# Optimization experiments

Measured on AMD Instinct MI355X. Metric: run time of the kernel, lower is better.

The kernel has to match this reference:

```python
import jax, jax.numpy as jnp
import numpy as np

D_MODEL = 1024
N_HEADS = 16
D_K = D_MODEL // N_HEADS
THETA = 10000.0
MAX_SEQ = 2048


def _trunc_normal(key, shape, std):
    # approximate trunc_normal in [-3std, 3std] via clipping (init only; values irrelevant to math)
    return jnp.clip(jax.random.normal(key, shape) * std, -3 * std, 3 * std).astype(jnp.float32)


def setup_inputs() -> dict:
    key = jax.random.key(0)
    kx, kq, kk, kv, ko = jax.random.split(key, 5)
    std = np.sqrt(2.0 / (D_MODEL + D_MODEL))
    x = jax.random.normal(kx, (2, 2048, D_MODEL), dtype=jnp.float32)
    W_q = _trunc_normal(kq, (D_MODEL, D_MODEL), std)
    W_k = _trunc_normal(kk, (D_MODEL, D_MODEL), std)
    W_v = _trunc_normal(kv, (D_MODEL, D_MODEL), std)
    W_o = _trunc_normal(ko, (D_MODEL, D_MODEL), std)
    return {"x": x, "W_q": W_q, "W_k": W_k, "W_v": W_v, "W_o": W_o}


def _rope(x, positions):
    # x: [b, n, s, d_k]; interleaved even/odd pairing: (x0,x1),(x2,x3),...
    d = x.shape[-1]
    inv_freq = THETA ** (-2.0 * jnp.arange(0, d // 2, dtype=jnp.float32) / d)
    angles = positions.astype(jnp.float32)[:, None] * inv_freq[None, :]  # [s, d/2]
    cos, sin = jnp.cos(angles), jnp.sin(angles)
    xp = x.reshape(x.shape[:-1] + (d // 2, 2))
    x_even, x_odd = xp[..., 0], xp[..., 1]
    out_even = x_even * cos - x_odd * sin
    out_odd = x_even * sin + x_odd * cos
    return jnp.stack((out_even, out_odd), axis=-1).reshape(x.shape)


def reference(x, W_q, W_k, W_v, W_o):
    b, s, _ = x.shape
    def split_heads(t):
        return t.reshape(b, s, N_HEADS, D_K).transpose(0, 2, 1, 3)  # b n s d
    Q = split_heads(x @ W_q.T)
    K = split_heads(x @ W_k.T)
    V = split_heads(x @ W_v.T)
    pos = jnp.arange(s)
    Q = _rope(Q, pos)
    K = _rope(K, pos)
    score = jnp.einsum('bnqd,bnkd->bnqk', Q, K) / jnp.sqrt(jnp.float32(D_K))
    causal = jnp.triu(jnp.ones((s, s), dtype=bool), k=1)
    score = jnp.where(causal[None, None], -jnp.inf, score)
    attn = jax.nn.softmax(score, axis=-1)
    out = jnp.einsum('bnqk,bnkd->bnqd', attn, V)
    out = out.transpose(0, 2, 1, 3).reshape(b, s, D_MODEL)
    return out @ W_o.T
```

## Files before the change

### kernel.cpp

```cpp
#include <hip/hip_runtime.h>

typedef float f32x4 __attribute__((ext_vector_type(4)));
typedef __bf16 bf16x8 __attribute__((ext_vector_type(8)));

#define D_MODEL 1024
#define SEQ     2048
#define NB      2
#define NH      16
#define DK      64

__device__ __forceinline__ unsigned short f2bf(float f) {
    union { float f; unsigned int u; } un; un.f = f;
    unsigned int r = un.u + 0x7fffu + ((un.u >> 16) & 1u);
    return (unsigned short)(r >> 16);
}

__device__ __forceinline__ unsigned cvtpk(float lo, float hi) {
    unsigned r;
    asm("v_cvt_pk_bf16_f32 %0, %1, %2" : "=v"(r) : "v"(lo), "v"(hi));
    return r;
}

__device__ __forceinline__ void gload16(const void* g, void* l) {
    __builtin_amdgcn_global_load_lds((__attribute__((address_space(1))) void*)g,
                                     (__attribute__((address_space(3))) void*)l,
                                     16, 0, 0);
}

__global__ __launch_bounds__(256) void cast5(
    const float* __restrict__ x,  const float* __restrict__ wq,
    const float* __restrict__ wk, const float* __restrict__ wv,
    const float* __restrict__ wo,
    unsigned short* __restrict__ xb,  unsigned short* __restrict__ wqb,
    unsigned short* __restrict__ wkb, unsigned short* __restrict__ wvb,
    unsigned short* __restrict__ wob, float2* __restrict__ tab)
{
    if (blockIdx.y == 5) {
        int idx = blockIdx.x * 256 + threadIdx.x;
        if (idx < SEQ * 32) {
            int ss = idx >> 5, p = idx & 31;
            float freq = exp2f(-0.41524101186f * (float)p);
            float sn, cs;
            sincosf((float)ss * freq, &sn, &cs);
            tab[idx] = make_float2(cs, sn);
        }
        return;
    }
    const float* src; unsigned short* dst; int n8;
    switch (blockIdx.y) {
        case 0:  src = x;  dst = xb;  n8 = (NB*SEQ*D_MODEL)/8; break;
        case 1:  src = wq; dst = wqb; n8 = (D_MODEL*D_MODEL)/8; break;
        case 2:  src = wk; dst = wkb; n8 = (D_MODEL*D_MODEL)/8; break;
        case 3:  src = wv; dst = wvb; n8 = (D_MODEL*D_MODEL)/8; break;
        default: src = wo; dst = wob; n8 = (D_MODEL*D_MODEL)/8; break;
    }
    int stride = gridDim.x * blockDim.x;
    for (int i = blockIdx.x * blockDim.x + threadIdx.x; i < n8; i += stride) {
        const float4* p = (const float4*)src + (size_t)i * 2;
        float4 a = p[0], b = p[1];
        union { unsigned short h[8]; uint4 v; } u;
        u.h[0] = f2bf(a.x); u.h[1] = f2bf(a.y); u.h[2] = f2bf(a.z); u.h[3] = f2bf(a.w);
        u.h[4] = f2bf(b.x); u.h[5] = f2bf(b.y); u.h[6] = f2bf(b.z); u.h[7] = f2bf(b.w);
        ((uint4*)dst)[i] = u.v;
    }
}

template <int MODE, int BM, int BN>
__global__ __launch_bounds__(256) void gemm_bt(
    const unsigned short* __restrict__ A,
    const unsigned short* __restrict__ B0,
    const unsigned short* __restrict__ B1,
    const unsigned short* __restrict__ B2,
    float* __restrict__ outF,
    unsigned short* __restrict__ Qh,
    unsigned short* __restrict__ Kh,
    unsigned short* __restrict__ Vt,
    const float2* __restrict__ tab,
    int M, int K)
{
    constexpr int PER_STAGE = (BM + BN) / 64;
    constexpr int WM = BM / 2, WN = BN / 2;
    constexpr int FM = WM / 16, FN = WN / 16;
    __shared__ __align__(16) unsigned short SM[3 * (BM + BN) * 32];

    const int lane = threadIdx.x & 63;
    const int wid  = threadIdx.x >> 6;
    const int l15 = lane & 15, lhi = lane >> 4;

    const int L  = blockIdx.x;
    const int yl = L & 7;
    const int t  = L >> 3;
    const int bx = t & 7;
    const int t2 = t >> 3;
    int y, z;
    if constexpr (MODE == 1) { y = ((t2 & 3) << 3) | yl; z = t2 >> 2; }
    else                     { y = (t2 << 3) | yl;       z = 0;       }
    const int m0 = y * BM;
    const int n0 = bx * BN;
    const unsigned short* B = (z == 0) ? B0 : (z == 1) ? B1 : B2;
    const int waveM = (wid >> 1) * WM;
    const int waveN = (wid & 1) * WN;

    f32x4 acc[FM][FN];
    f32x4 zero = {0.f, 0.f, 0.f, 0.f};
#pragma unroll
    for (int m = 0; m < FM; ++m)
#pragma unroll
        for (int n = 0; n < FN; ++n) acc[m][n] = zero;

    const int lrow = lane >> 2;
    const int uslot = lane & 3;

    auto STAGE = [&](int buf, int k0) {
        unsigned short* as = SM + buf * (BM + BN) * 32;
        unsigned short* bs = as + BM * 32;
#pragma unroll
        for (int q = 0; q < BM / 64; ++q) {
            int rbase = wid * (BM / 4) + q * 16;
            int r = rbase + lrow;
            int ug = (uslot - (r >> 1)) & 3;
            gload16(A + (size_t)(m0 + r) * K + k0 + ug * 8,
                    (char*)as + rbase * 64);
        }
#pragma unroll
        for (int q = 0; q < BN / 64; ++q) {
            int rbase = wid * (BN / 4) + q * 16;
            int r = rbase + lrow;
            int ug = (uslot - (r >> 1)) & 3;
            gload16(B + (size_t)(n0 + r) * K + k0 + ug * 8,
                    (char*)bs + rbase * 64);
        }
    };

    const int NK = K >> 5;
    STAGE(0, 0);
    STAGE(1, 32);

    for (int k = 0; k < NK; ++k) {
        if (k < NK - 1) {
            if constexpr (PER_STAGE == 4) asm volatile("s_waitcnt vmcnt(4)" ::: "memory");
            else                          asm volatile("s_waitcnt vmcnt(3)" ::: "memory");
        } else {
            asm volatile("s_waitcnt vmcnt(0)" ::: "memory");
        }
        __builtin_amdgcn_s_barrier();
        __builtin_amdgcn_sched_barrier(0);
        if (k + 2 < NK) STAGE((k + 2) % 3, (k + 2) << 5);

        const unsigned short* as = SM + (k % 3) * (BM + BN) * 32;
        const unsigned short* bs = as + BM * 32;
        bf16x8 af[FM], bfr[FN];
#pragma unroll
        for (int m = 0; m < FM; ++m) {
            int ra = waveM + m * 16 + l15;
            af[m] = *(const bf16x8*)(as + ra * 32 + (((lhi + (ra >> 1)) & 3) << 3));
        }
#pragma unroll
        for (int n = 0; n < FN; ++n) {
            int rb = waveN + n * 16 + l15;
            bfr[n] = *(const bf16x8*)(bs + rb * 32 + (((lhi + (rb >> 1)) & 3) << 3));
        }
        __builtin_amdgcn_s_setprio(1);
#pragma unroll
        for (int m = 0; m < FM; ++m)
#pragma unroll
            for (int n = 0; n < FN; ++n)
                acc[m][n] = __builtin_amdgcn_mfma_f32_16x16x32_bf16(af[m], bfr[n], acc[m][n], 0, 0, 0);
        __builtin_amdgcn_s_setprio(0);
    }

    if constexpr (MODE == 0) {
#pragma unroll
        for (int n = 0; n < FN; ++n) {
            int col = n0 + waveN + n * 16 + l15;
#pragma unroll
            for (int m = 0; m < FM; ++m) {
                int rowb = m0 + waveM + m * 16 + (lhi << 2);
#pragma unroll
                for (int r = 0; r < 4; ++r)
                    outF[(size_t)(rowb + r) * D_MODEL + col] = acc[m][n][r];
            }
        }
    } else {
        __syncthreads();
        unsigned short* Ct = ((unsigned short*)SM) + wid * 4608;
        const int colg0 = n0 + waveN;
        const int hh    = (colg0 >> 6) & (NH - 1);
        const int rowg0 = m0 + waveM;
        const int bb    = rowg0 >> 11;
        const size_t bhh = (size_t)(bb * NH + hh);

#pragma unroll
        for (int n = 0; n < 4; ++n) {
            int cl = n * 16 + l15;
#pragma unroll
            for (int m = 0; m < 4; ++m) {
#pragma unroll
                for (int r = 0; r < 4; ++r) {
                    float v  = acc[m][n][r];
                    float pv = __shfl_xor(v, 1);
                    int rl = m * 16 + (lhi << 2) + r;
                    if (z == 2) {
                        Ct[cl * 72 + rl] = f2bf(v);
                    } else {
                        int ss = (rowg0 + rl) & (SEQ - 1);
                        float2 cs = tab[(ss << 5) + (cl >> 1)];
                        float o = (cl & 1) ? (pv * cs.y + v * cs.x)
                                           : (v * cs.x - pv * cs.y);
                        if (z == 0) o *= 0.18033688011f;
                        Ct[rl * 72 + cl] = f2bf(o);
                    }
                }
            }
        }
        asm volatile("s_waitcnt lgkmcnt(0)" ::: "memory");

        const int lr = lane >> 3;
        const int lc = (lane & 7) << 3;
#pragma unroll
        for (int i = 0; i < 8; ++i) {
            int rl = i * 8 + lr;
            uint4 w = *(const uint4*)&Ct[rl * 72 + lc];
            if (z == 2) {
                int ss0 = rowg0 & (SEQ - 1);
                *(uint4*)(Vt + (bhh * DK + rl) * SEQ + ss0 + lc) = w;
            } else {
                int ss = (rowg0 + rl) & (SEQ - 1);
                unsigned short* dst = (z == 0) ? Qh : Kh;
                *(uint4*)(dst + (bhh * SEQ + ss) * DK + lc) = w;
            }
        }
    }
}

__global__ __launch_bounds__(256) void attn_kernel(
    const unsigned short* __restrict__ Qh,
    const unsigned short* __restrict__ Kh,
    const unsigned short* __restrict__ Vt,
    unsigned short* __restrict__ O)
{
    __shared__ unsigned short Ks[3][64 * 64];
    __shared__ unsigned short Vs[3][64 * 64];
    __shared__ unsigned short P[4][16 * 64];

    const int tid  = threadIdx.x;
    const int lane = tid & 63;
    const int wid  = tid >> 6;
    const int l15 = lane & 15, lhi = lane >> 4;

    const int L   = blockIdx.x;
    const int xcd = L & 7;
    const int r0  = L >> 3;
    const int bh  = (xcd << 2) | (r0 & 3);
    const int pi  = r0 >> 2;
    const int b = bh >> 4, h = bh & 15;

    const unsigned short* Qb = Qh + (size_t)bh * SEQ * DK;
    const unsigned short* Kb = Kh + (size_t)bh * SEQ * DK;
    const unsigned short* Vb = Vt + (size_t)bh * DK * SEQ;

    const int NT0 = pi + 1;
    const int NTT = 33;

    auto kv_of = [&](int g) { return (g < NT0 ? g : g - NT0) << 6; };

    auto STAGE = [&](int buf, int kv0s) {
#pragma unroll
        for (int c = 0; c < 2; ++c) {
            int ub = c * 256 + wid * 64;
            int u  = ub + lane;
            int kr = u >> 3;
            int kc = (u & 7) ^ (kr & 7);
            gload16(Kb + (size_t)(kv0s + kr) * DK + kc * 8, &Ks[buf][(size_t)ub * 8]);
            gload16(Vb + (size_t)kr * SEQ + kv0s + kc * 8, &Vs[buf][(size_t)ub * 8]);
        }
    };

    const f32x4 zero = {0.f, 0.f, 0.f, 0.f};
    const f32x4 ninf = {-1e30f, -1e30f, -1e30f, -1e30f};
    const int sw = l15 & 7;

    STAGE(0, 0);
    STAGE(1, kv_of(1));
    int g = 0;

    for (int ph = 0; ph < 2; ++ph) {
        const int qt = ph ? (31 - pi) : pi;
        const int q0 = qt << 6;
        const int qw = q0 + wid * 16;
        const int lastkt = qt;

        bf16x8 qf[2];
#pragma unroll
        for (int kk = 0; kk < 2; ++kk)
            qf[kk] = *(const bf16x8*)(Qb + (size_t)(qw + l15) * DK + kk * 32 + lhi * 8);

        f32x4 oacc[4];
#pragma unroll
        for (int nd = 0; nd < 4; ++nd) oacc[nd] = zero;
        float mrow = -1e30f;
        float lrow = 0.f;

        for (int kt = 0; kt <= lastkt; ++kt, ++g) {
            const int kv0 = kt << 6;
            const bool diag = (kt == lastkt);
            const int nlim = diag ? (wid + 1) : 4;

            if (g < NTT - 1) asm volatile("s_waitcnt vmcnt(4)" ::: "memory");
            else             asm volatile("s_waitcnt vmcnt(0)" ::: "memory");
            __builtin_amdgcn_s_barrier();
            __builtin_amdgcn_sched_barrier(0);
            if (g + 2 < NTT) STAGE((g + 2) % 3, kv_of(g + 2));

            const unsigned short* Kc = Ks[g % 3];
            const unsigned short* Vc = Vs[g % 3];

            f32x4 s[4];
#pragma unroll
            for (int n = 0; n < 4; ++n) s[n] = (n < nlim) ? zero : ninf;

            __builtin_amdgcn_s_setprio(1);
#pragma unroll
            for (int n = 0; n < 4; ++n) {
                if (n < nlim) {
                    int rr = n * 16 + l15;
                    bf16x8 k0 = *(const bf16x8*)&Kc[rr * 64 + ((lhi ^ sw) << 3)];
                    bf16x8 k1 = *(const bf16x8*)&Kc[rr * 64 + (((4 + lhi) ^ sw) << 3)];
                    s[n] = __builtin_amdgcn_mfma_f32_16x16x32_bf16(k0, qf[0], s[n], 0, 0, 0);
                    s[n] = __builtin_amdgcn_mfma_f32_16x16x32_bf16(k1, qf[1], s[n], 0, 0, 0);
                }
            }
            __builtin_amdgcn_s_setprio(0);

            if (diag) {
                const int qg = qw + l15;
#pragma unroll
                for (int n = 0; n < 4; ++n) {
                    if (n < nlim) {
#pragma unroll
                        for (int rr = 0; rr < 4; ++rr) {
                            int kg = kv0 + n * 16 + (lhi << 2) + rr;
                            if (kg > qg) s[n][rr] = -1e30f;
                        }
                    }
                }
            }

            float mx = fmaxf(fmaxf(s[0][0], s[0][1]), fmaxf(s[0][2], s[0][3]));
#pragma unroll
            for (int n = 1; n < 4; ++n)
                mx = fmaxf(mx, fmaxf(fmaxf(s[n][0], s[n][1]), fmaxf(s[n][2], s[n][3])));
            mx = fmaxf(mx, __shfl_xor(mx, 16));
            mx = fmaxf(mx, __shfl_xor(mx, 32));

            float alpha = 1.f;
            const int allDefer = __all(mx <= mrow + 8.f);
            if (!allDefer) {
                float mn = fmaxf(mrow, mx);
                alpha = __builtin_amdgcn_exp2f(mrow - mn);
                mrow = mn;
            }

#pragma unroll
            for (int n = 0; n < 4; ++n)
#pragma unroll
                for (int rr = 0; rr < 4; ++rr)
                    s[n][rr] = __builtin_amdgcn_exp2f(s[n][rr] - mrow);

            float rs = 0.f;
#pragma unroll
            for (int n = 0; n < 4; ++n)
                rs += (s[n][0] + s[n][1]) + (s[n][2] + s[n][3]);
            rs += __shfl_xor(rs, 16);
            rs += __shfl_xor(rs, 32);
            lrow = allDefer ? (lrow + rs) : (lrow * alpha + rs);

#pragma unroll
            for (int n = 0; n < 4; ++n) {
                uint2 pk;
                pk.x = cvtpk(s[n][0], s[n][1]);
                pk.y = cvtpk(s[n][2], s[n][3]);
                int cW = 2 * n + (lhi >> 1);
                *(uint2*)&P[wid][(l15 << 6) + ((cW ^ sw) << 3) + ((lhi & 1) << 2)] = pk;
            }

            if (!allDefer) {
                float a0 = __shfl(alpha, (lhi << 2) + 0);
                float a1 = __shfl(alpha, (lhi << 2) + 1);
                float a2 = __shfl(alpha, (lhi << 2) + 2);
                float a3 = __shfl(alpha, (lhi << 2) + 3);
#pragma unroll
                for (int nd = 0; nd < 4; ++nd) {
                    oacc[nd][0] *= a0; oacc[nd][1] *= a1;
                    oacc[nd][2] *= a2; oacc[nd][3] *= a3;
                }
            }

            asm volatile("s_waitcnt lgkmcnt(0)" ::: "memory");
            const int kklim = diag ? ((nlim + 1) >> 1) : 2;
            bf16x8 pa[2];
#pragma unroll
            for (int kk = 0; kk < 2; ++kk)
                if (kk < kklim)
                    pa[kk] = *(const bf16x8*)&P[wid][(l15 << 6) + ((((kk << 2) + lhi) ^ sw) << 3)];

            __builtin_amdgcn_s_setprio(1);
#pragma unroll
            for (int nd = 0; nd < 4; ++nd)
#pragma unroll
                for (int kk = 0; kk < 2; ++kk)
                    if (kk < kklim) {
                        int rd = nd * 16 + l15;
                        bf16x8 vf = *(const bf16x8*)&Vc[rd * 64 + ((((kk << 2) + lhi) ^ sw) << 3)];
                        oacc[nd] = __builtin_amdgcn_mfma_f32_16x16x32_bf16(pa[kk], vf, oacc[nd], 0, 0, 0);
                    }
            __builtin_amdgcn_s_setprio(0);
        }

        float inv = 1.f / lrow;
        float i0 = __shfl(inv, (lhi << 2) + 0);
        float i1 = __shfl(inv, (lhi << 2) + 1);
        float i2 = __shfl(inv, (lhi << 2) + 2);
        float i3 = __shfl(inv, (lhi << 2) + 3);
#pragma unroll
        for (int nd = 0; nd < 4; ++nd) {
            int d = nd * 16 + l15;
            int rowb = qw + (lhi << 2);
            O[((size_t)(b * SEQ + rowb + 0)) * D_MODEL + h * DK + d] = f2bf(oacc[nd][0] * i0);
            O[((size_t)(b * SEQ + rowb + 1)) * D_MODEL + h * DK + d] = f2bf(oacc[nd][1] * i1);
            O[((size_t)(b * SEQ + rowb + 2)) * D_MODEL + h * DK + d] = f2bf(oacc[nd][2] * i2);
            O[((size_t)(b * SEQ + rowb + 3)) * D_MODEL + h * DK + d] = f2bf(oacc[nd][3] * i3);
        }
    }
}

extern "C" void kernel_launch(void* const* d_in, const int* in_sizes, int n_in,
                              void* d_out, int out_size, void* d_ws, size_t ws_size,
                              hipStream_t stream)
{
    const float* x  = (const float*)d_in[0];
    const float* Wq = (const float*)d_in[1];
    const float* Wk = (const float*)d_in[2];
    const float* Wv = (const float*)d_in[3];
    const float* Wo = (const float*)d_in[4];
    float* out = (float*)d_out;

    char* ws = (char*)d_ws;
    unsigned short* xb  = (unsigned short*)(ws);
    unsigned short* Wqb = (unsigned short*)(ws + ( 8ull << 20));
    unsigned short* Wkb = (unsigned short*)(ws + (10ull << 20));
    unsigned short* Wvb = (unsigned short*)(ws + (12ull << 20));
    unsigned short* Wob = (unsigned short*)(ws + (14ull << 20));
    unsigned short* Qh  = (unsigned short*)(ws + (16ull << 20));
    unsigned short* Kh  = (unsigned short*)(ws + (24ull << 20));
    unsigned short* Vt  = (unsigned short*)(ws + (32ull << 20));
    float2*         tab = (float2*)(ws + (40ull << 20));
    unsigned short* attn = xb;

    cast5<<<dim3(512, 6), 256, 0, stream>>>(x, Wq, Wk, Wv, Wo, xb, Wqb, Wkb, Wvb, Wob, tab);

    gemm_bt<1, 128, 128><<<768, 256, 0, stream>>>(
        xb, Wqb, Wkb, Wvb, nullptr, Qh, Kh, Vt, tab, NB * SEQ, D_MODEL);

    attn_kernel<<<512, 256, 0, stream>>>(Qh, Kh, Vt, attn);

    gemm_bt<0, 64, 128><<<512, 256, 0, stream>>>(
        attn, Wob, Wob, Wob, out, nullptr, nullptr, nullptr, nullptr, NB * SEQ, D_MODEL);
}
```

Before: 116.2 us.

## Split long causal query tiles across two blocks with partial-softmax merge kernel

The attention grid doubles from 512 to 1024 blocks. Each long query tile (rows 16..31) is now split across the two blocks of a pair: each computes a partial KV range and writes unnormalized fp32 output plus (max, sum) to scratch, and a new merge kernel combines them with log-sum-exp rescaling. Each block does about 16-17 KV tiles, which balances work and raises occupancy. The K/V staging also drops from triple to double buffering with a full vmcnt(0) wait, and the launch pays for an extra kernel plus fp32 partial traffic. One partial buffer lives in the output tensor before the final GEMM overwrites it.

```diff
diff --git a/kernel.cpp b/kernel.cpp
--- a/kernel.cpp
+++ b/kernel.cpp
@@ -237,10 +237,12 @@
     const unsigned short* __restrict__ Qh,
     const unsigned short* __restrict__ Kh,
     const unsigned short* __restrict__ Vt,
-    unsigned short* __restrict__ O)
+    unsigned short* __restrict__ O,
+    float* __restrict__ paO, float2* __restrict__ paM,
+    float* __restrict__ pbO, float2* __restrict__ pbM)
 {
-    __shared__ unsigned short Ks[3][64 * 64];
-    __shared__ unsigned short Vs[3][64 * 64];
+    __shared__ unsigned short Ks[2][64 * 64];
+    __shared__ unsigned short Vs[2][64 * 64];
     __shared__ unsigned short P[4][16 * 64];
 
     const int tid  = threadIdx.x;
@@ -248,23 +250,29 @@
     const int wid  = tid >> 6;
     const int l15 = lane & 15, lhi = lane >> 4;
 
-    const int L   = blockIdx.x;
-    const int xcd = L & 7;
-    const int r0  = L >> 3;
-    const int bh  = (xcd << 2) | (r0 & 3);
-    const int pi  = r0 >> 2;
+    const int L    = blockIdx.x;
+    const int xcd  = L & 7;
+    const int r0   = L >> 3;
+    const int bh   = (xcd << 2) | (r0 & 3);
+    const int rest = r0 >> 2;
+    const int pi   = rest & 15;
+    const int j    = rest >> 4;
     const int b = bh >> 4, h = bh & 15;
+    const size_t p = (size_t)bh * 16 + (15 - pi);
 
     const unsigned short* Qb = Qh + (size_t)bh * SEQ * DK;
     const unsigned short* Kb = Kh + (size_t)bh * SEQ * DK;
     const unsigned short* Vb = Vt + (size_t)bh * DK * SEQ;
 
-    const int NT0 = pi + 1;
-    const int NTT = 33;
-
-    auto kv_of = [&](int g) { return (g < NT0 ? g : g - NT0) << 6; };
-
-    auto STAGE = [&](int buf, int kv0s) {
+    const int NT = j ? 16 : 17;
+
+    auto kv_of = [&](int g) {
+        if (j) return 16 - pi + g;
+        return (g <= pi) ? g : g - (pi + 1);
+    };
+
+    auto STAGE = [&](int buf, int kvt) {
+        int kv0s = kvt << 6;
 #pragma unroll
         for (int c = 0; c < 2; ++c) {
             int ub = c * 256 + wid * 64;
@@ -280,15 +288,18 @@
     const f32x4 ninf = {-1e30f, -1e30f, -1e30f, -1e30f};
     const int sw = l15 & 7;
 
-    STAGE(0, 0);
-    STAGE(1, kv_of(1));
+    STAGE(0, kv_of(0));
     int g = 0;
 
-    for (int ph = 0; ph < 2; ++ph) {
-        const int qt = ph ? (31 - pi) : pi;
+    const int nph = j ? 1 : 2;
+    for (int ph = 0; ph < nph; ++ph) {
+        int qt, ktbeg, ktend, dodiag, finalw;
+        if (j == 0 && ph == 0) { qt = pi;      ktbeg = 0;       ktend = pi;      dodiag = 1; finalw = 1; }
+        else if (j == 0)       { qt = 31 - pi; ktbeg = 0;       ktend = 15 - pi; dodiag = 0; finalw = 0; }
+        else                   { qt = 31 - pi; ktbeg = 16 - pi; ktend = 31 - pi; dodiag = 1; finalw = 0; }
+
         const int q0 = qt << 6;
         const int qw = q0 + wid * 16;
-        const int lastkt = qt;
 
         bf16x8 qf[2];
 #pragma unroll
@@ -301,19 +312,18 @@
         float mrow = -1e30f;
         float lrow = 0.f;
 
-        for (int kt = 0; kt <= lastkt; ++kt, ++g) {
+        for (int kt = ktbeg; kt <= ktend; ++kt, ++g) {
             const int kv0 = kt << 6;
-            const bool diag = (kt == lastkt);
+            const bool diag = dodiag && (kt == ktend);
             const int nlim = diag ? (wid + 1) : 4;
 
-            if (g < NTT - 1) asm volatile("s_waitcnt vmcnt(4)" ::: "memory");
-            else             asm volatile("s_waitcnt vmcnt(0)" ::: "memory");
+            asm volatile("s_waitcnt vmcnt(0)" ::: "memory");
             __builtin_amdgcn_s_barrier();
             __builtin_amdgcn_sched_barrier(0);
-            if (g + 2 < NTT) STAGE((g + 2) % 3, kv_of(g + 2));
-
-            const unsigned short* Kc = Ks[g % 3];
-            const unsigned short* Vc = Vs[g % 3];
+            if (g + 1 < NT) STAGE((g + 1) & 1, kv_of(g + 1));
+
+            const unsigned short* Kc = Ks[g & 1];
+            const unsigned short* Vc = Vs[g & 1];
 
             f32x4 s[4];
 #pragma unroll
@@ -417,21 +427,67 @@
             __builtin_amdgcn_s_setprio(0);
         }
 
-        float inv = 1.f / lrow;
-        float i0 = __shfl(inv, (lhi << 2) + 0);
-        float i1 = __shfl(inv, (lhi << 2) + 1);
-        float i2 = __shfl(inv, (lhi << 2) + 2);
-        float i3 = __shfl(inv, (lhi << 2) + 3);
-#pragma unroll
-        for (int nd = 0; nd < 4; ++nd) {
-            int d = nd * 16 + l15;
-            int rowb = qw + (lhi << 2);
-            O[((size_t)(b * SEQ + rowb + 0)) * D_MODEL + h * DK + d] = f2bf(oacc[nd][0] * i0);
-            O[((size_t)(b * SEQ + rowb + 1)) * D_MODEL + h * DK + d] = f2bf(oacc[nd][1] * i1);
-            O[((size_t)(b * SEQ + rowb + 2)) * D_MODEL + h * DK + d] = f2bf(oacc[nd][2] * i2);
-            O[((size_t)(b * SEQ + rowb + 3)) * D_MODEL + h * DK + d] = f2bf(oacc[nd][3] * i3);
+        if (finalw) {
+            float inv = 1.f / lrow;
+            float i0 = __shfl(inv, (lhi << 2) + 0);
+            float i1 = __shfl(inv, (lhi << 2) + 1);
+            float i2 = __shfl(inv, (lhi << 2) + 2);
+            float i3 = __shfl(inv, (lhi << 2) + 3);
+#pragma unroll
+            for (int nd = 0; nd < 4; ++nd) {
+                int d = nd * 16 + l15;
+                int rowb = qw + (lhi << 2);
+                O[((size_t)(b * SEQ + rowb + 0)) * D_MODEL + h * DK + d] = f2bf(oacc[nd][0] * i0);
+                O[((size_t)(b * SEQ + rowb + 1)) * D_MODEL + h * DK + d] = f2bf(oacc[nd][1] * i1);
+                O[((size_t)(b * SEQ + rowb + 2)) * D_MODEL + h * DK + d] = f2bf(oacc[nd][2] * i2);
+                O[((size_t)(b * SEQ + rowb + 3)) * D_MODEL + h * DK + d] = f2bf(oacc[nd][3] * i3);
+            }
+        } else {
+            float*  PO = (j ? pbO : paO) + p * 4096;
+            float2* PM = (j ? pbM : paM) + p * 64;
+#pragma unroll
+            for (int nd = 0; nd < 4; ++nd)
+#pragma unroll
+                for (int rr = 0; rr < 4; ++rr) {
+                    int rowl = wid * 16 + (lhi << 2) + rr;
+                    PO[rowl * 64 + nd * 16 + l15] = oacc[nd][rr];
+                }
+            if (lhi == 0)
+                PM[wid * 16 + l15] = make_float2(mrow, lrow);
         }
     }
+}
+
+__global__ __launch_bounds__(256) void attn_merge(
+    const float* __restrict__ paO, const float2* __restrict__ paM,
+    const float* __restrict__ pbO, const float2* __restrict__ pbM,
+    unsigned short* __restrict__ O)
+{
+    const int mb = blockIdx.x;
+    const int bh = mb >> 4, qq = mb & 15;
+    const int b = bh >> 4, h = bh & 15;
+    const int q0 = (16 + qq) << 6;
+    const size_t p = (size_t)bh * 16 + qq;
+    const int t = threadIdx.x;
+    const int r = t >> 2;
+    const int c0 = (t & 3) << 4;
+
+    float2 ma = paM[p * 64 + r];
+    float2 mbv = pbM[p * 64 + r];
+    float m = fmaxf(ma.x, mbv.x);
+    float a1 = __builtin_amdgcn_exp2f(ma.x - m);
+    float a2 = __builtin_amdgcn_exp2f(mbv.x - m);
+    float inv = 1.f / (ma.y * a1 + mbv.y * a2);
+
+    const float* o1 = paO + p * 4096 + r * 64 + c0;
+    const float* o2 = pbO + p * 4096 + r * 64 + c0;
+    union { unsigned short hh[16]; uint4 v[2]; } u;
+#pragma unroll
+    for (int c = 0; c < 16; ++c)
+        u.hh[c] = f2bf((o1[c] * a1 + o2[c] * a2) * inv);
+    uint4* dst = (uint4*)(O + ((size_t)(b * SEQ + q0 + r)) * D_MODEL + h * DK + c0);
+    dst[0] = u.v[0];
+    dst[1] = u.v[1];
 }
 
 extern "C" void kernel_launch(void* const* d_in, const int* in_sizes, int n_in,
@@ -457,12 +513,18 @@
     float2*         tab = (float2*)(ws + (40ull << 20));
     unsigned short* attn = xb;
 
+    float*  paO = out;
+    float2* paM = (float2*)(out + 512 * 4096);
+    float*  pbO = (float*)(ws + (41ull << 20));
+    float2* pbM = (float2*)(ws + (49ull << 20));
+
     cast5<<<dim3(512, 6), 256, 0, stream>>>(x, Wq, Wk, Wv, Wo, xb, Wqb, Wkb, Wvb, Wob, tab);
 
     gemm_bt<1, 128, 128><<<768, 256, 0, stream>>>(
         xb, Wqb, Wkb, Wvb, nullptr, Qh, Kh, Vt, tab, NB * SEQ, D_MODEL);
 
-    attn_kernel<<<512, 256, 0, stream>>>(Qh, Kh, Vt, attn);
+    attn_kernel<<<1024, 256, 0, stream>>>(Qh, Kh, Vt, attn, paO, paM, pbO, pbM);
+    attn_merge<<<512, 256, 0, stream>>>(paO, paM, pbO, pbM, attn);
 
     gemm_bt<0, 64, 128><<<512, 256, 0, stream>>>(
         attn, Wob, Wob, Wob, out, nullptr, nullptr, nullptr, nullptr, NB * SEQ, D_MODEL);
```

Result: no change. 117.2 us (+0.9%).
